# Performance work log

Hardware: AMD Instinct MI355X
Metric: run time of the kernel (lower is better)

The kernel has to match this reference:

```python
import jax, jax.numpy as jnp
import numpy as np

B, P, G, C = 64, 5000, 300, 20   # images, preds/img, gt/img, num classes
INPUT_SIZE = 512.0
IOU_THRESH = 0.5


def setup_inputs() -> dict:
    key = jax.random.key(0)
    k1, k2, k3, k4, k5, k6, k7 = jax.random.split(key, 7)
    # predictions: [x1,y1,x2,y2,score,cls], boxes normalized to [0,1]
    pxy = jax.random.uniform(k1, (B, P, 2), minval=0.0, maxval=0.8)
    pwh = jax.random.uniform(k2, (B, P, 2), minval=0.02, maxval=0.2)
    score = jax.random.uniform(k3, (B, P, 1))
    pcls = jax.random.randint(k4, (B, P, 1), 0, C).astype(jnp.float32)
    output = jnp.concatenate([pxy, pxy + pwh, score, pcls], axis=-1)
    # ground truth: [x1,y1,x2,y2,cls]
    txy = jax.random.uniform(k5, (B, G, 2), minval=0.0, maxval=0.8)
    twh = jax.random.uniform(k6, (B, G, 2), minval=0.02, maxval=0.2)
    tcls = jax.random.randint(k7, (B, G, 1), 0, C).astype(jnp.float32)
    labels = jnp.concatenate([txy, txy + twh, tcls], axis=-1)
    return {"output": output, "labels": labels}


def reference(output, labels):
    scale = jnp.array([INPUT_SIZE, INPUT_SIZE, INPUT_SIZE, INPUT_SIZE], dtype=output.dtype)

    def match_image(preds, targets):  # preds [P,6], targets [G,5]
        tcls = targets[:, 4]
        tboxes = targets[:, :4] * scale                     # [G,4]
        tarea = (tboxes[:, 2] - tboxes[:, 0]) * (tboxes[:, 3] - tboxes[:, 1])

        def step(detected, pred):
            pbox = pred[:4] * scale
            lt = jnp.maximum(pbox[:2], tboxes[:, :2])       # [G,2]
            rb = jnp.minimum(pbox[2:], tboxes[:, 2:])
            wh = jnp.clip(rb - lt, 0.0)
            inter = wh[:, 0] * wh[:, 1]
            parea = (pbox[2] - pbox[0]) * (pbox[3] - pbox[1])
            ious = inter / (parea + tarea - inter)          # [G]
            cls_mask = tcls == pred[5]
            masked = jnp.where(cls_mask, ious, -1.0)
            bi = jnp.argmax(masked)                          # greedy argmax over same-class gt
            match = ((pred[4] > 0)
                     & jnp.any(cls_mask)
                     & (masked[bi] > IOU_THRESH)
                     & (~detected[bi]))                      # sequential dedup
            detected = detected.at[bi].set(detected[bi] | match)
            return detected, match

        _, correct = jax.lax.scan(step, jnp.zeros(tboxes.shape[0], dtype=bool), preds)
        return correct                                       # [P] bool

    correct = jax.vmap(match_image)(output, labels).astype(output.dtype)  # [B,P]
    # stats: (correct flag, score, predicted class) per prediction; tcls per image
    stats = jnp.stack([correct, output[:, :, 4], output[:, :, 5]], axis=-1)  # [B,P,3]
    tcls = labels[:, :, 4]                                                    # [B,G]
    return stats, tcls
```

## Files before the change

### kernel.cpp

```cpp
#include <hip/hip_runtime.h>
#include <cstdint>

#define B 64
#define P 5000
#define G 300
#define C 20
#define SCALE_F 512.0f
#define IOU_TH 0.5f
#define NSPLIT 8
#define PCHUNK ((P + NSPLIT - 1) / NSPLIT)
#define NTA 512
#define NWAVE (NTA / 64)
#define SPT ((PCHUNK + NTA - 1) / NTA)
#define NPCH (SPT * NWAVE)
#define NCHUNK ((G + 63) / 64)
#define SENT 0x7FFFFFFF

#pragma clang fp contract(off)

__global__ __launch_bounds__(NTA, 4) void match_kernel(
    const float* __restrict__ preds,
    const float* __restrict__ labels,
    int* __restrict__ blockfp,
    float* __restrict__ out_stats,
    float* __restrict__ out_tcls)
{
    const int s = blockIdx.x;
    const int b = blockIdx.y;
    const int tid = threadIdx.x;
    const int lane = tid & 63;
    const int w = tid >> 6;

    __shared__ float  plds[PCHUNK * 6];
    __shared__ float4 sb[G];
    __shared__ float  sa[G];
    __shared__ short  ssi[G];
    __shared__ int    chist[NCHUNK][C];
    __shared__ int    phist[NPCH][C];
    __shared__ int    so[C + 1];
    __shared__ int    firstp[G];
    __shared__ unsigned short psorted[PCHUNK];

    const float* lab = labels + (size_t)b * G * 5;
    const float* prd = preds + (size_t)b * P * 6;
    const int pbase = s * PCHUNK;
    const int pend = (pbase + PCHUNK < P) ? pbase + PCHUNK : P;
    const int npred = pend - pbase;

    if (tid < G) firstp[tid] = SENT;

    float tx1 = 0, ty1 = 0, tx2 = 0, ty2 = 0;
    int tc = -1;
    unsigned long long tmask = 0;
    if (tid < NCHUNK * 64) {
        if (tid < G) {
            tx1 = lab[tid * 5 + 0];
            ty1 = lab[tid * 5 + 1];
            tx2 = lab[tid * 5 + 2];
            ty2 = lab[tid * 5 + 3];
            float cf = lab[tid * 5 + 4];
            tc = (int)cf;
            if (s == 0) out_tcls[(size_t)b * G + tid] = cf;
        }
        #pragma unroll
        for (int cc = 0; cc < C; ++cc) {
            unsigned long long m = __ballot(tc == cc);
            if (tc == cc) tmask = m;
            if (lane == cc) chist[w][cc] = __popcll(m);
        }
    }

    for (int i = tid; i < npred * 6; i += NTA)
        plds[i] = prd[(size_t)pbase * 6 + i];

    int myc[SPT];
    unsigned long long pmask[SPT];
    #pragma unroll
    for (int k = 0; k < SPT; ++k) {
        myc[k] = -1;
        pmask[k] = 0;
        int p = pbase + k * NTA + tid;
        if (p < pend) {
            float2 sc = *reinterpret_cast<const float2*>(prd + (size_t)p * 6 + 4);
            myc[k] = (int)sc.y;
            size_t ip3 = ((size_t)b * P + p) * 3;
            out_stats[ip3 + 0] = 0.0f;
            out_stats[ip3 + 1] = sc.x;
            out_stats[ip3 + 2] = sc.y;
        }
        #pragma unroll
        for (int cc = 0; cc < C; ++cc) {
            unsigned long long m = __ballot(myc[k] == cc);
            if (myc[k] == cc) pmask[k] = m;
            if (lane == cc) phist[k * NWAVE + w][cc] = __popcll(m);
        }
    }
    __syncthreads();

    if (tid < 64) {
        int run = 0;
        if (lane < C) {
            #pragma unroll
            for (int u = 0; u < NCHUNK; ++u) {
                int t = chist[u][lane]; chist[u][lane] = run; run += t;
            }
        }
        int v = (lane < C) ? run : 0;
        #pragma unroll
        for (int d = 1; d < 32; d <<= 1) {
            int o = __shfl_up(v, d);
            if (lane >= d) v += o;
        }
        if (lane < C) so[lane + 1] = v;
        if (lane == 0) so[0] = 0;
    } else if (tid < 128) {
        int run = 0;
        if (lane < C) {
            #pragma unroll
            for (int u = 0; u < NPCH; ++u) {
                int t = phist[u][lane]; phist[u][lane] = run; run += t;
            }
        }
        int v = (lane < C) ? run : 0;
        #pragma unroll
        for (int d = 1; d < 32; d <<= 1) {
            int o = __shfl_up(v, d);
            if (lane >= d) v += o;
        }
        int excl = v - run;
        if (lane < C) {
            #pragma unroll
            for (int u = 0; u < NPCH; ++u) phist[u][lane] += excl;
        }
    }
    __syncthreads();

    if (tid < G) {
        int rank = chist[w][tc] + __popcll(tmask & ((1ull << lane) - 1));
        int pos = so[tc] + rank;
        float x1 = tx1 * SCALE_F;
        float y1 = ty1 * SCALE_F;
        float x2 = tx2 * SCALE_F;
        float y2 = ty2 * SCALE_F;
        sb[pos] = make_float4(x1, y1, x2, y2);
        sa[pos] = (x2 - x1) * (y2 - y1);
        ssi[pos] = (short)tid;
    }
    #pragma unroll
    for (int k = 0; k < SPT; ++k) {
        if (myc[k] >= 0) {
            int pos = phist[k * NWAVE + w][myc[k]]
                    + __popcll(pmask[k] & ((1ull << lane) - 1));
            psorted[pos] = (unsigned short)(k * NTA + tid);
        }
    }
    __syncthreads();

    #pragma unroll
    for (int k = 0; k < SPT; ++k) {
        int slot = k * NTA + tid;
        if (slot >= npred) continue;
        int li = psorted[slot];
        const float* pp = &plds[li * 6];
        float2 q0 = *reinterpret_cast<const float2*>(pp);
        float2 q1 = *reinterpret_cast<const float2*>(pp + 2);
        float2 q2 = *reinterpret_cast<const float2*>(pp + 4);
        float px1 = q0.x * SCALE_F;
        float py1 = q0.y * SCALE_F;
        float px2 = q1.x * SCALE_F;
        float py2 = q1.y * SCALE_F;
        float score = q2.x;
        int c = (int)q2.y;
        float parea = (px2 - px1) * (py2 - py1);

        int lo = so[c], hi = so[c + 1];
        float best = -1.0f;
        int bi = -1;
        for (int j = lo; j < hi; ++j) {
            float4 tb = sb[j];
            float lx = fmaxf(px1, tb.x);
            float ly = fmaxf(py1, tb.y);
            float rx = fminf(px2, tb.z);
            float ry = fminf(py2, tb.w);
            float wd = fmaxf(rx - lx, 0.0f);
            float ht = fmaxf(ry - ly, 0.0f);
            float inter = wd * ht;
            float uni = (parea + sa[j]) - inter;
            float iou = inter / uni;
            if (iou > best) { best = iou; bi = ssi[j]; }
        }

        bool eligible = (score > 0.0f) && (hi > lo) && (best > IOU_TH);
        if (eligible) atomicMin(&firstp[bi], pbase + li);
    }
    __syncthreads();

    if (tid < G)
        blockfp[((size_t)b * NSPLIT + s) * G + tid] = firstp[tid];
}

__global__ __launch_bounds__(512) void resolve_kernel(
    const int* __restrict__ blockfp,
    float* __restrict__ out_stats)
{
    const int b = blockIdx.x;
    const int t = threadIdx.x;
    if (t >= G) return;

    const int* fp = blockfp + (size_t)b * NSPLIT * G + t;
    int m = fp[0];
    #pragma unroll
    for (int s = 1; s < NSPLIT; ++s) m = min(m, fp[s * G]);

    if (m != SENT)
        out_stats[((size_t)b * P + m) * 3] = 1.0f;
}

extern "C" void kernel_launch(void* const* d_in, const int* in_sizes, int n_in,
                              void* d_out, int out_size, void* d_ws, size_t ws_size,
                              hipStream_t stream) {
    const float* output = (const float*)d_in[0];
    const float* labels = (const float*)d_in[1];

    float* out_stats = (float*)d_out;
    float* out_tcls  = (float*)d_out + (size_t)B * P * 3;

    int* blockfp = (int*)d_ws;

    dim3 grid(NSPLIT, B);
    match_kernel<<<grid, NTA, 0, stream>>>(output, labels, blockfp,
                                           out_stats, out_tcls);
    resolve_kernel<<<dim3(B), 512, 0, stream>>>(blockfp, out_stats);
}
```

Measured before the change: 73.87 us.

## Fuse match and resolve into one block-per-image kernel with atomic class sort

```diff
diff --git a/kernel.cpp b/kernel.cpp
--- a/kernel.cpp
+++ b/kernel.cpp
@@ -7,12 +7,9 @@
 #define C 20
 #define SCALE_F 512.0f
 #define IOU_TH 0.5f
-#define NSPLIT 8
-#define PCHUNK ((P + NSPLIT - 1) / NSPLIT)
-#define NTA 512
+#define NTA 1024
 #define NWAVE (NTA / 64)
-#define SPT ((PCHUNK + NTA - 1) / NTA)
-#define NPCH (SPT * NWAVE)
+#define SPT ((P + NTA - 1) / NTA)
 #define NCHUNK ((G + 63) / 64)
 #define SENT 0x7FFFFFFF
 
@@ -21,32 +18,27 @@
 __global__ __launch_bounds__(NTA, 4) void match_kernel(
     const float* __restrict__ preds,
     const float* __restrict__ labels,
-    int* __restrict__ blockfp,
     float* __restrict__ out_stats,
     float* __restrict__ out_tcls)
 {
-    const int s = blockIdx.x;
-    const int b = blockIdx.y;
+    const int b = blockIdx.x;
     const int tid = threadIdx.x;
     const int lane = tid & 63;
     const int w = tid >> 6;
 
-    __shared__ float  plds[PCHUNK * 6];
     __shared__ float4 sb[G];
     __shared__ float  sa[G];
     __shared__ short  ssi[G];
     __shared__ int    chist[NCHUNK][C];
-    __shared__ int    phist[NPCH][C];
     __shared__ int    so[C + 1];
+    __shared__ int    pcnt[C];
     __shared__ int    firstp[G];
-    __shared__ unsigned short psorted[PCHUNK];
+    __shared__ unsigned short psorted[P];
 
     const float* lab = labels + (size_t)b * G * 5;
     const float* prd = preds + (size_t)b * P * 6;
-    const int pbase = s * PCHUNK;
-    const int pend = (pbase + PCHUNK < P) ? pbase + PCHUNK : P;
-    const int npred = pend - pbase;
 
+    if (tid < C) pcnt[tid] = 0;
     if (tid < G) firstp[tid] = SENT;
 
     float tx1 = 0, ty1 = 0, tx2 = 0, ty2 = 0;
@@ -60,7 +52,7 @@
             ty2 = lab[tid * 5 + 3];
             float cf = lab[tid * 5 + 4];
             tc = (int)cf;
-            if (s == 0) out_tcls[(size_t)b * G + tid] = cf;
+            out_tcls[(size_t)b * G + tid] = cf;
         }
         #pragma unroll
         for (int cc = 0; cc < C; ++cc) {
@@ -70,17 +62,12 @@
         }
     }
 
-    for (int i = tid; i < npred * 6; i += NTA)
-        plds[i] = prd[(size_t)pbase * 6 + i];
-
     int myc[SPT];
-    unsigned long long pmask[SPT];
     #pragma unroll
     for (int k = 0; k < SPT; ++k) {
         myc[k] = -1;
-        pmask[k] = 0;
-        int p = pbase + k * NTA + tid;
-        if (p < pend) {
+        int p = k * NTA + tid;
+        if (p < P) {
             float2 sc = *reinterpret_cast<const float2*>(prd + (size_t)p * 6 + 4);
             myc[k] = (int)sc.y;
             size_t ip3 = ((size_t)b * P + p) * 3;
@@ -88,13 +75,12 @@
             out_stats[ip3 + 1] = sc.x;
             out_stats[ip3 + 2] = sc.y;
         }
-        #pragma unroll
-        for (int cc = 0; cc < C; ++cc) {
-            unsigned long long m = __ballot(myc[k] == cc);
-            if (myc[k] == cc) pmask[k] = m;
-            if (lane == cc) phist[k * NWAVE + w][cc] = __popcll(m);
-        }
     }
+    __syncthreads();
+
+    #pragma unroll
+    for (int k = 0; k < SPT; ++k)
+        if (myc[k] >= 0) atomicAdd(&pcnt[myc[k]], 1);
     __syncthreads();
 
     if (tid < 64) {
@@ -113,25 +99,10 @@
         }
         if (lane < C) so[lane + 1] = v;
         if (lane == 0) so[0] = 0;
-    } else if (tid < 128) {
-        int run = 0;
-        if (lane < C) {
-            #pragma unroll
-            for (int u = 0; u < NPCH; ++u) {
-                int t = phist[u][lane]; phist[u][lane] = run; run += t;
-            }
-        }
-        int v = (lane < C) ? run : 0;
-        #pragma unroll
-        for (int d = 1; d < 32; d <<= 1) {
-            int o = __shfl_up(v, d);
-            if (lane >= d) v += o;
-        }
-        int excl = v - run;
-        if (lane < C) {
-            #pragma unroll
-            for (int u = 0; u < NPCH; ++u) phist[u][lane] += excl;
-        }
+    }
+    if (tid == 64) {
+        int a = 0;
+        for (int c = 0; c < C; ++c) { int v = pcnt[c]; pcnt[c] = a; a += v; }
     }
     __syncthreads();
 
@@ -148,10 +119,10 @@
     }
     #pragma unroll
     for (int k = 0; k < SPT; ++k) {
-        if (myc[k] >= 0) {
-            int pos = phist[k * NWAVE + w][myc[k]]
-                    + __popcll(pmask[k] & ((1ull << lane) - 1));
-            psorted[pos] = (unsigned short)(k * NTA + tid);
+        int p = k * NTA + tid;
+        if (p < P) {
+            int pos = atomicAdd(&pcnt[myc[k]], 1);
+            psorted[pos] = (unsigned short)p;
         }
     }
     __syncthreads();
@@ -159,12 +130,12 @@
     #pragma unroll
     for (int k = 0; k < SPT; ++k) {
         int slot = k * NTA + tid;
-        if (slot >= npred) continue;
-        int li = psorted[slot];
-        const float* pp = &plds[li * 6];
-        float2 q0 = *reinterpret_cast<const float2*>(pp);
-        float2 q1 = *reinterpret_cast<const float2*>(pp + 2);
-        float2 q2 = *reinterpret_cast<const float2*>(pp + 4);
+        if (slot >= P) continue;
+        int p = psorted[slot];
+        const float* pr = prd + (size_t)p * 6;
+        float2 q0 = *reinterpret_cast<const float2*>(pr);
+        float2 q1 = *reinterpret_cast<const float2*>(pr + 2);
+        float2 q2 = *reinterpret_cast<const float2*>(pr + 4);
         float px1 = q0.x * SCALE_F;
         float py1 = q0.y * SCALE_F;
         float px2 = q1.x * SCALE_F;
@@ -191,29 +162,15 @@
         }
 
         bool eligible = (score > 0.0f) && (hi > lo) && (best > IOU_TH);
-        if (eligible) atomicMin(&firstp[bi], pbase + li);
+        if (eligible) atomicMin(&firstp[bi], p);
     }
     __syncthreads();
 
-    if (tid < G)
-        blockfp[((size_t)b * NSPLIT + s) * G + tid] = firstp[tid];
-}
-
-__global__ __launch_bounds__(512) void resolve_kernel(
-    const int* __restrict__ blockfp,
-    float* __restrict__ out_stats)
-{
-    const int b = blockIdx.x;
-    const int t = threadIdx.x;
-    if (t >= G) return;
-
-    const int* fp = blockfp + (size_t)b * NSPLIT * G + t;
-    int m = fp[0];
-    #pragma unroll
-    for (int s = 1; s < NSPLIT; ++s) m = min(m, fp[s * G]);
-
-    if (m != SENT)
-        out_stats[((size_t)b * P + m) * 3] = 1.0f;
+    if (tid < G) {
+        int m = firstp[tid];
+        if (m != SENT)
+            out_stats[((size_t)b * P + m) * 3] = 1.0f;
+    }
 }
 
 extern "C" void kernel_launch(void* const* d_in, const int* in_sizes, int n_in,
@@ -225,10 +182,6 @@
     float* out_stats = (float*)d_out;
     float* out_tcls  = (float*)d_out + (size_t)B * P * 3;
 
-    int* blockfp = (int*)d_ws;
-
-    dim3 grid(NSPLIT, B);
-    match_kernel<<<grid, NTA, 0, stream>>>(output, labels, blockfp,
-                                           out_stats, out_tcls);
-    resolve_kernel<<<dim3(B), 512, 0, stream>>>(blockfp, out_stats);
+    match_kernel<<<dim3(B), NTA, 0, stream>>>(output, labels,
+                                              out_stats, out_tcls);
 }
```

New measurement: 81.06 us. 1.1x slower.
